# Kernel tuning notes

Measured on AMD Instinct MI355X. Metric: run time of the kernel, lower is better.

The kernel has to match this reference:

```python
import jax, jax.numpy as jnp
import numpy as np

H = 256          # LSTM hidden size
P = 1            # proj_size
L = 5            # num LSTM layers
T = 1000         # sequence length (forced by Linear(1000, 100))


def _uniform(key, shape, scale):
    return jax.random.uniform(key, shape, dtype=jnp.float32, minval=-scale, maxval=scale)


def setup_inputs() -> dict:
    key = jax.random.key(0)
    ks = jax.random.split(key, 16)
    B = 128
    s = 1.0 / np.sqrt(H)  # PyTorch LSTM init scale
    inp = {
        "x": jax.random.normal(ks[0], (B, T, 1), dtype=jnp.float32),
        # stacked LSTM params: layer input dim is 1 for all layers (input_size=1, proj_size=1)
        "Wih": _uniform(ks[1], (L, 4 * H, 1), s),
        "Whh": _uniform(ks[2], (L, 4 * H, P), s),
        "bih": _uniform(ks[3], (L, 4 * H), s),
        "bhh": _uniform(ks[4], (L, 4 * H), s),
        "Whr": _uniform(ks[5], (L, P, H), s),
        # MLP head
        "W1": _uniform(ks[6], (100, 1000), 1.0 / np.sqrt(1000)),
        "b1": _uniform(ks[7], (100,), 1.0 / np.sqrt(1000)),
        "W2": _uniform(ks[8], (100, 100), 0.1),
        "b2": _uniform(ks[9], (100,), 0.1),
        "W3": _uniform(ks[10], (100, 100), 0.1),
        "b3": _uniform(ks[11], (100,), 0.1),
        "W4": _uniform(ks[12], (1, 100), 0.1),
        "b4": _uniform(ks[13], (1,), 0.1),
    }
    return inp


def _lstm_layer(x_seq, Wih, Whh, bih, bhh, Whr):
    """One projected LSTM layer. x_seq: [B, T, in_dim] -> [B, T, P]."""
    B = x_seq.shape[0]
    # precompute input contribution for all timesteps: [B, T, 4H]
    gx = jnp.einsum('bti,gi->btg', x_seq, Wih) + bih + bhh
    gx = jnp.transpose(gx, (1, 0, 2))  # [T, B, 4H] for scan

    def step(carry, g_t):
        h, c = carry                      # h: [B, P], c: [B, H]
        gates = g_t + h @ Whh.T           # [B, 4H]
        i = jax.nn.sigmoid(gates[:, 0 * H:1 * H])
        f = jax.nn.sigmoid(gates[:, 1 * H:2 * H])
        g = jnp.tanh(gates[:, 2 * H:3 * H])
        o = jax.nn.sigmoid(gates[:, 3 * H:4 * H])
        c = f * c + i * g
        h = (o * jnp.tanh(c)) @ Whr.T     # projected hidden: [B, P]
        return (h, c), h

    h0 = jnp.zeros((B, P), x_seq.dtype)
    c0 = jnp.zeros((B, H), x_seq.dtype)
    _, hs = jax.lax.scan(step, (h0, c0), gx)  # hs: [T, B, P]
    return jnp.transpose(hs, (1, 0, 2))       # [B, T, P]


def reference(x, Wih, Whh, bih, bhh, Whr, W1, b1, W2, b2, W3, b3, W4, b4):
    out = x
    for l in range(L):  # fixed 5 stacked layers
        out = _lstm_layer(out, Wih[l], Whh[l], bih[l], bhh[l], Whr[l])
    out = out[:, :, 0]                      # squeeze -> [B, 1000]
    out = jax.nn.sigmoid(out @ W1.T + b1)   # linear1 + Sigmoid
    out = jax.nn.sigmoid(out @ W2.T + b2)   # linear2 + Sigmoid
    out = jax.nn.relu(out @ W3.T + b3)      # linear3 + ReLU
    out = out @ W4.T + b4                   # linear4 -> [B, 1]
    return out
```

## Files before the change

kernel.cpp:

```cpp
#include <hip/hip_runtime.h>


#define LAYERS 5
#define TT 1000
#define BATCH 128
#define CH 40
#define NCH (TT / CH)

#define LOG2E 1.4426950408889634f

__device__ __forceinline__ float fast_exp2(float x) {
#if __has_builtin(__builtin_amdgcn_exp2f)
  return __builtin_amdgcn_exp2f(x);
#else
  return __exp2f(x);
#endif
}
__device__ __forceinline__ float fast_rcp(float x) {
#if __has_builtin(__builtin_amdgcn_rcpf)
  return __builtin_amdgcn_rcpf(x);
#else
  return 1.0f / x;
#endif
}
__device__ __forceinline__ float fast_sigmoid(float z) {
  float e = fast_exp2(-LOG2E * z);
  return fast_rcp(1.0f + e);
}

template <int CTRL>
__device__ __forceinline__ float dpp_add(float v) {
  int moved = __builtin_amdgcn_update_dpp(0, __builtin_bit_cast(int, v),
                                          CTRL, 0xF, 0xF, false);
  return v + __builtin_bit_cast(float, moved);
}

__device__ __forceinline__ float wave_sum_uniform(float v) {
  v = dpp_add<0x128>(v);
  v = dpp_add<0x124>(v);
  v = dpp_add<0x122>(v);
  v = dpp_add<0x121>(v);
  v = dpp_add<0x142>(v);
  v = dpp_add<0x143>(v);
  return __builtin_bit_cast(float, __builtin_amdgcn_readlane(__builtin_bit_cast(int, v), 63));
}

__device__ __forceinline__ float lane_bcast(float v, int s) {
  return __builtin_bit_cast(float, __builtin_amdgcn_readlane(__builtin_bit_cast(int, v), s));
}

__global__ __launch_bounds__(64) void lstm_wave_kernel(
    const float* __restrict__ x,
    const float* __restrict__ Wih,
    const float* __restrict__ Whh,
    const float* __restrict__ bih,
    const float* __restrict__ bhh,
    const float* __restrict__ Whr,
    float* __restrict__ seq,
    int* __restrict__ flags)
{
  const int bid  = blockIdx.x;
  const int l    = bid >> 7;
  const int b    = bid & 127;
  const int lane = threadIdx.x;

  float wix[4][4], whx[4][4], gb[4][4], whr[4], cc[4];
  const int base = l * 1024;
#pragma unroll
  for (int g = 0; g < 4; ++g) {
    const float sc = (g == 2) ? (-2.0f * LOG2E) : (-LOG2E);
#pragma unroll
    for (int k = 0; k < 4; ++k) {
      int j = base + g * 256 + k * 64 + lane;
      wix[g][k] = Wih[j] * sc;
      whx[g][k] = Whh[j] * sc;
      gb[g][k]  = (bih[j] + bhh[j]) * sc;
    }
  }
#pragma unroll
  for (int k = 0; k < 4; ++k) {
    whr[k] = Whr[l * 256 + k * 64 + lane];
    cc[k] = 0.0f;
  }

  const float* in  = (l == 0) ? (x + b * TT) : (seq + ((l - 1) * BATCH + b) * TT);
  float*       out = seq + (l * BATCH + b) * TT;
  int*       my_flag = flags + l * BATCH + b;
  const int* in_flag = (l > 0) ? (flags + (l - 1) * BATCH + b) : (const int*)flags;

  float h = 0.0f;
  for (int c = 0; c < NCH; ++c) {
    if (l > 0) {
      while (__hip_atomic_load(in_flag, __ATOMIC_ACQUIRE,
                               __HIP_MEMORY_SCOPE_AGENT) <= c)
        __builtin_amdgcn_s_sleep(2);
    }
    float xv = 0.0f;
    if (lane < CH) {
      if (l == 0)
        xv = in[c * CH + lane];
      else
        xv = __hip_atomic_load(in + c * CH + lane, __ATOMIC_RELAXED,
                               __HIP_MEMORY_SCOPE_AGENT);
    }

    float outv = 0.0f;
#pragma unroll 2
    for (int s = 0; s < CH; ++s) {
      const float xs = lane_bcast(xv, s);

      float gx[4][4];
#pragma unroll
      for (int g = 0; g < 4; ++g)
#pragma unroll
        for (int k = 0; k < 4; ++k)
          gx[g][k] = fmaf(xs, wix[g][k], gb[g][k]);

      float E[4][4];
#pragma unroll
      for (int g = 0; g < 4; ++g)
#pragma unroll
        for (int k = 0; k < 4; ++k)
          E[g][k] = fast_exp2(fmaf(h, whx[g][k], gx[g][k]));

      float r0, r1, r2, r3;
      {
        float rr[4];
#pragma unroll
        for (int k = 0; k < 4; ++k) {
          float ig = fast_rcp(1.0f + E[0][k]);
          float fg = fast_rcp(1.0f + E[1][k]);
          float gg = fmaf(2.0f, fast_rcp(1.0f + E[2][k]), -1.0f);
          float og = fast_rcp(1.0f + E[3][k]);
          cc[k] = fmaf(fg, cc[k], ig * gg);
          float tE = fast_exp2(cc[k] * (-2.0f * LOG2E));
          float tc = fmaf(2.0f, fast_rcp(1.0f + tE), -1.0f);
          rr[k] = og * tc * whr[k];
        }
        r0 = rr[0]; r1 = rr[1]; r2 = rr[2]; r3 = rr[3];
      }
      float r = (r0 + r1) + (r2 + r3);

      h = wave_sum_uniform(r);
      if (lane == s) outv = h;
    }

    if (l < 4) {
      if (lane < CH)
        __hip_atomic_store(out + c * CH + lane, outv, __ATOMIC_RELAXED,
                           __HIP_MEMORY_SCOPE_AGENT);
      if (lane == 0)
        __hip_atomic_store(my_flag, c + 1, __ATOMIC_RELEASE,
                           __HIP_MEMORY_SCOPE_AGENT);
    } else {
      if (lane < CH) out[c * CH + lane] = outv;
    }
  }
}

__global__ __launch_bounds__(256) void mlp_head_kernel(
    const float* __restrict__ seq4,
    const float* __restrict__ W1, const float* __restrict__ b1,
    const float* __restrict__ W2, const float* __restrict__ b2,
    const float* __restrict__ W3, const float* __restrict__ b3,
    const float* __restrict__ W4, const float* __restrict__ b4,
    float* __restrict__ out)
{
  __shared__ float sx[TT];
  __shared__ float sh[100];
  __shared__ float sh2[100];
  __shared__ float part[100];
  __shared__ float red[4];

  const int b = blockIdx.x, tid = threadIdx.x;
  for (int i = tid; i < TT; i += 256) sx[i] = seq4[b * TT + i];
  __syncthreads();

  const int half = (tid >= 128) ? 1 : 0;
  const int oid  = half ? (tid - 128) : tid;
  float myacc = 0.0f;
  if (oid < 100) {
    const float* w  = W1 + oid * TT + half * 500;
    const float* xx = sx + half * 500;
    float a0 = 0.f, a1 = 0.f, a2 = 0.f, a3 = 0.f;
    for (int t0 = 0; t0 < 500; t0 += 4) {
      float4 v = *(const float4*)(w + t0);
      a0 = fmaf(v.x, xx[t0 + 0], a0);
      a1 = fmaf(v.y, xx[t0 + 1], a1);
      a2 = fmaf(v.z, xx[t0 + 2], a2);
      a3 = fmaf(v.w, xx[t0 + 3], a3);
    }
    myacc = (a0 + a1) + (a2 + a3);
    if (half) part[oid] = myacc;
  }
  __syncthreads();
  if (tid < 100) sh[tid] = fast_sigmoid(myacc + part[tid] + b1[tid]);
  __syncthreads();

  if (tid < 100) {
    float acc = b2[tid];
    const float* w = W2 + tid * 100;
    for (int k = 0; k < 100; ++k) acc += w[k] * sh[k];
    sh2[tid] = fast_sigmoid(acc);
  }
  __syncthreads();

  if (tid < 100) {
    float acc = b3[tid];
    const float* w = W3 + tid * 100;
    for (int k = 0; k < 100; ++k) acc += w[k] * sh2[k];
    sh[tid] = fmaxf(acc, 0.0f);
  }
  __syncthreads();

  float r = (tid < 100) ? sh[tid] * W4[tid] : 0.0f;
  {
    r = dpp_add<0x128>(r);
    r = dpp_add<0x124>(r);
    r = dpp_add<0x122>(r);
    r = dpp_add<0x121>(r);
    r = dpp_add<0x142>(r);
    r = dpp_add<0x143>(r);
    r = __builtin_bit_cast(float, __builtin_amdgcn_readlane(__builtin_bit_cast(int, r), 63));
  }
  if ((tid & 63) == 0) red[tid >> 6] = r;
  __syncthreads();
  if (tid == 0) out[b] = (red[0] + red[1]) + (red[2] + red[3]) + b4[0];
}

extern "C" void kernel_launch(void* const* d_in, const int* in_sizes, int n_in,
                              void* d_out, int out_size, void* d_ws, size_t ws_size,
                              hipStream_t stream) {
  const float* x   = (const float*)d_in[0];
  const float* Wih = (const float*)d_in[1];
  const float* Whh = (const float*)d_in[2];
  const float* bih = (const float*)d_in[3];
  const float* bhh = (const float*)d_in[4];
  const float* Whr = (const float*)d_in[5];
  const float* W1  = (const float*)d_in[6];
  const float* b1  = (const float*)d_in[7];
  const float* W2  = (const float*)d_in[8];
  const float* b2  = (const float*)d_in[9];
  const float* W3  = (const float*)d_in[10];
  const float* b3  = (const float*)d_in[11];
  const float* W4  = (const float*)d_in[12];
  const float* b4  = (const float*)d_in[13];

  float* seq   = (float*)d_ws;
  int*   flags = (int*)(seq + LAYERS * BATCH * TT);

  hipMemsetAsync(flags, 0, LAYERS * BATCH * sizeof(int), stream);
  lstm_wave_kernel<<<LAYERS * BATCH, 64, 0, stream>>>(x, Wih, Whh, bih, bhh, Whr,
                                                      seq, flags);
  mlp_head_kernel<<<BATCH, 256, 0, stream>>>(seq + 4 * BATCH * TT,
                                             W1, b1, W2, b2, W3, b3, W4, b4,
                                             (float*)d_out);
}
```

Before: 562.3 us.

## Spread each LSTM cell across four waves and fuse MLP head into layer-4 blocks

```diff
diff --git a/kernel.cpp b/kernel.cpp
--- a/kernel.cpp
+++ b/kernel.cpp
@@ -35,58 +35,70 @@
   return v + __builtin_bit_cast(float, moved);
 }
 
-__device__ __forceinline__ float wave_sum_uniform(float v) {
+__device__ __forceinline__ float wave_sum_hi(float v) {
   v = dpp_add<0x128>(v);
   v = dpp_add<0x124>(v);
   v = dpp_add<0x122>(v);
   v = dpp_add<0x121>(v);
   v = dpp_add<0x142>(v);
   v = dpp_add<0x143>(v);
-  return __builtin_bit_cast(float, __builtin_amdgcn_readlane(__builtin_bit_cast(int, v), 63));
+  return v;
 }
 
 __device__ __forceinline__ float lane_bcast(float v, int s) {
   return __builtin_bit_cast(float, __builtin_amdgcn_readlane(__builtin_bit_cast(int, v), s));
 }
 
-__global__ __launch_bounds__(64) void lstm_wave_kernel(
+__global__ __launch_bounds__(256) void lstm_fused_kernel(
     const float* __restrict__ x,
     const float* __restrict__ Wih,
     const float* __restrict__ Whh,
     const float* __restrict__ bih,
     const float* __restrict__ bhh,
     const float* __restrict__ Whr,
+    const float* __restrict__ W1, const float* __restrict__ b1,
+    const float* __restrict__ W2, const float* __restrict__ b2,
+    const float* __restrict__ W3, const float* __restrict__ b3,
+    const float* __restrict__ W4, const float* __restrict__ b4,
+    float* __restrict__ out,
     float* __restrict__ seq,
     int* __restrict__ flags)
 {
+  __shared__ __align__(16) float part[2][4];
+  __shared__ float sx[TT];
+  __shared__ float sh[100];
+  __shared__ float sh2[100];
+  __shared__ float partm[100];
+  __shared__ float red[4];
+
   const int bid  = blockIdx.x;
   const int l    = bid >> 7;
   const int b    = bid & 127;
-  const int lane = threadIdx.x;
-
-  float wix[4][4], whx[4][4], gb[4][4], whr[4], cc[4];
+  const int tid  = threadIdx.x;
+  const int wid  = tid >> 6;
+  const int lane = tid & 63;
+  const int e    = tid;
+
+  float wix[4], whx[4], gb[4];
   const int base = l * 1024;
 #pragma unroll
   for (int g = 0; g < 4; ++g) {
     const float sc = (g == 2) ? (-2.0f * LOG2E) : (-LOG2E);
-#pragma unroll
-    for (int k = 0; k < 4; ++k) {
-      int j = base + g * 256 + k * 64 + lane;
-      wix[g][k] = Wih[j] * sc;
-      whx[g][k] = Whh[j] * sc;
-      gb[g][k]  = (bih[j] + bhh[j]) * sc;
-    }
-  }
-#pragma unroll
-  for (int k = 0; k < 4; ++k) {
-    whr[k] = Whr[l * 256 + k * 64 + lane];
-    cc[k] = 0.0f;
-  }
-
-  const float* in  = (l == 0) ? (x + b * TT) : (seq + ((l - 1) * BATCH + b) * TT);
-  float*       out = seq + (l * BATCH + b) * TT;
+    int j = base + g * 256 + e;
+    wix[g] = Wih[j] * sc;
+    whx[g] = Whh[j] * sc;
+    gb[g]  = (bih[j] + bhh[j]) * sc;
+  }
+  const float whr = Whr[l * 256 + e];
+  float cc = 0.0f;
+
+  const float* in   = (l == 0) ? (x + b * TT) : (seq + ((l - 1) * BATCH + b) * TT);
+  float*       outp = seq + (l * BATCH + b) * TT;
   int*       my_flag = flags + l * BATCH + b;
   const int* in_flag = (l > 0) ? (flags + (l - 1) * BATCH + b) : (const int*)flags;
+
+  const float M4 = -4.0f * LOG2E;
+  const float P2 =  2.0f * LOG2E;
 
   float h = 0.0f;
   for (int c = 0; c < NCH; ++c) {
@@ -97,11 +109,9 @@
     }
     float xv = 0.0f;
     if (lane < CH) {
-      if (l == 0)
-        xv = in[c * CH + lane];
-      else
-        xv = __hip_atomic_load(in + c * CH + lane, __ATOMIC_RELAXED,
-                               __HIP_MEMORY_SCOPE_AGENT);
+      xv = (l == 0) ? in[c * CH + lane]
+                    : __hip_atomic_load(in + c * CH + lane, __ATOMIC_RELAXED,
+                                        __HIP_MEMORY_SCOPE_AGENT);
     }
 
     float outv = 0.0f;
@@ -109,71 +119,45 @@
     for (int s = 0; s < CH; ++s) {
       const float xs = lane_bcast(xv, s);
 
-      float gx[4][4];
-#pragma unroll
-      for (int g = 0; g < 4; ++g)
-#pragma unroll
-        for (int k = 0; k < 4; ++k)
-          gx[g][k] = fmaf(xs, wix[g][k], gb[g][k]);
-
-      float E[4][4];
-#pragma unroll
-      for (int g = 0; g < 4; ++g)
-#pragma unroll
-        for (int k = 0; k < 4; ++k)
-          E[g][k] = fast_exp2(fmaf(h, whx[g][k], gx[g][k]));
-
-      float r0, r1, r2, r3;
-      {
-        float rr[4];
-#pragma unroll
-        for (int k = 0; k < 4; ++k) {
-          float ig = fast_rcp(1.0f + E[0][k]);
-          float fg = fast_rcp(1.0f + E[1][k]);
-          float gg = fmaf(2.0f, fast_rcp(1.0f + E[2][k]), -1.0f);
-          float og = fast_rcp(1.0f + E[3][k]);
-          cc[k] = fmaf(fg, cc[k], ig * gg);
-          float tE = fast_exp2(cc[k] * (-2.0f * LOG2E));
-          float tc = fmaf(2.0f, fast_rcp(1.0f + tE), -1.0f);
-          rr[k] = og * tc * whr[k];
-        }
-        r0 = rr[0]; r1 = rr[1]; r2 = rr[2]; r3 = rr[3];
-      }
-      float r = (r0 + r1) + (r2 + r3);
-
-      h = wave_sum_uniform(r);
-      if (lane == s) outv = h;
-    }
-
-    if (l < 4) {
+      float p0 = fmaf(h, whx[0], fmaf(xs, wix[0], gb[0]));
+      float p1 = fmaf(h, whx[1], fmaf(xs, wix[1], gb[1]));
+      float p2 = fmaf(h, whx[2], fmaf(xs, wix[2], gb[2]));
+      float p3 = fmaf(h, whx[3], fmaf(xs, wix[3], gb[3]));
+      float E0 = fast_exp2(p0), E1 = fast_exp2(p1);
+      float E2 = fast_exp2(p2), E3 = fast_exp2(p3);
+      float R0 = fast_rcp(1.0f + E0);
+      float R1 = fast_rcp(1.0f + E1);
+      float R2 = fast_rcp(1.0f + E2);
+      float R3 = fast_rcp(1.0f + E3);
+      float gsc = fmaf(M4, R2, P2);
+      cc = fmaf(R1, cc, R0 * gsc);
+      float tR = fast_rcp(1.0f + fast_exp2(cc));
+      float ow = R3 * whr;
+      float r  = fmaf(ow + ow, tR, -ow);
+
+      float v = wave_sum_hi(r);
+      const int pr = s & 1;
+      if (lane == 63) part[pr][wid] = v;
+      __syncthreads();
+      const float4 pp = *(const float4*)part[pr];
+      h = (pp.x + pp.y) + (pp.z + pp.w);
+
+      if (wid == 0 && lane == s) outv = h;
+      if (l == 4 && tid == 0) sx[c * CH + s] = h;
+    }
+
+    if (l < 4 && wid == 0) {
       if (lane < CH)
-        __hip_atomic_store(out + c * CH + lane, outv, __ATOMIC_RELAXED,
+        __hip_atomic_store(outp + c * CH + lane, outv, __ATOMIC_RELAXED,
                            __HIP_MEMORY_SCOPE_AGENT);
       if (lane == 0)
         __hip_atomic_store(my_flag, c + 1, __ATOMIC_RELEASE,
                            __HIP_MEMORY_SCOPE_AGENT);
-    } else {
-      if (lane < CH) out[c * CH + lane] = outv;
-    }
-  }
-}
-
-__global__ __launch_bounds__(256) void mlp_head_kernel(
-    const float* __restrict__ seq4,
-    const float* __restrict__ W1, const float* __restrict__ b1,
-    const float* __restrict__ W2, const float* __restrict__ b2,
-    const float* __restrict__ W3, const float* __restrict__ b3,
-    const float* __restrict__ W4, const float* __restrict__ b4,
-    float* __restrict__ out)
-{
-  __shared__ float sx[TT];
-  __shared__ float sh[100];
-  __shared__ float sh2[100];
-  __shared__ float part[100];
-  __shared__ float red[4];
-
-  const int b = blockIdx.x, tid = threadIdx.x;
-  for (int i = tid; i < TT; i += 256) sx[i] = seq4[b * TT + i];
+    }
+  }
+
+  if (l != 4) return;
+
   __syncthreads();
 
   const int half = (tid >= 128) ? 1 : 0;
@@ -191,10 +175,10 @@
       a3 = fmaf(v.w, xx[t0 + 3], a3);
     }
     myacc = (a0 + a1) + (a2 + a3);
-    if (half) part[oid] = myacc;
-  }
-  __syncthreads();
-  if (tid < 100) sh[tid] = fast_sigmoid(myacc + part[tid] + b1[tid]);
+    if (half) partm[oid] = myacc;
+  }
+  __syncthreads();
+  if (tid < 100) sh[tid] = fast_sigmoid(myacc + partm[tid] + b1[tid]);
   __syncthreads();
 
   if (tid < 100) {
@@ -214,15 +198,13 @@
   __syncthreads();
 
   float r = (tid < 100) ? sh[tid] * W4[tid] : 0.0f;
-  {
-    r = dpp_add<0x128>(r);
-    r = dpp_add<0x124>(r);
-    r = dpp_add<0x122>(r);
-    r = dpp_add<0x121>(r);
-    r = dpp_add<0x142>(r);
-    r = dpp_add<0x143>(r);
-    r = __builtin_bit_cast(float, __builtin_amdgcn_readlane(__builtin_bit_cast(int, r), 63));
-  }
+  r = dpp_add<0x128>(r);
+  r = dpp_add<0x124>(r);
+  r = dpp_add<0x122>(r);
+  r = dpp_add<0x121>(r);
+  r = dpp_add<0x142>(r);
+  r = dpp_add<0x143>(r);
+  r = __builtin_bit_cast(float, __builtin_amdgcn_readlane(__builtin_bit_cast(int, r), 63));
   if ((tid & 63) == 0) red[tid >> 6] = r;
   __syncthreads();
   if (tid == 0) out[b] = (red[0] + red[1]) + (red[2] + red[3]) + b4[0];
@@ -250,9 +232,7 @@
   int*   flags = (int*)(seq + LAYERS * BATCH * TT);
 
   hipMemsetAsync(flags, 0, LAYERS * BATCH * sizeof(int), stream);
-  lstm_wave_kernel<<<LAYERS * BATCH, 64, 0, stream>>>(x, Wih, Whh, bih, bhh, Whr,
-                                                      seq, flags);
-  mlp_head_kernel<<<BATCH, 256, 0, stream>>>(seq + 4 * BATCH * TT,
-                                             W1, b1, W2, b2, W3, b3, W4, b4,
-                                             (float*)d_out);
-}
+  lstm_fused_kernel<<<LAYERS * BATCH, 256, 0, stream>>>(
+      x, Wih, Whh, bih, bhh, Whr, W1, b1, W2, b2, W3, b3, W4, b4,
+      (float*)d_out, seq, flags);
+}
```

Measured after the change: 843.6 us. 50.0% more time.

## Replace chunked flag handoff with per-timestep poisoned-value wavefront pipeline

Applied to the files above, without the earlier changes.

```diff
diff --git a/kernel.cpp b/kernel.cpp
--- a/kernel.cpp
+++ b/kernel.cpp
@@ -4,8 +4,7 @@
 #define LAYERS 5
 #define TT 1000
 #define BATCH 128
-#define CH 40
-#define NCH (TT / CH)
+#define POISON 0xFFFFFFFFu
 
 #define LOG2E 1.4426950408889634f
 
@@ -45,8 +44,8 @@
   return __builtin_bit_cast(float, __builtin_amdgcn_readlane(__builtin_bit_cast(int, v), 63));
 }
 
-__device__ __forceinline__ float lane_bcast(float v, int s) {
-  return __builtin_bit_cast(float, __builtin_amdgcn_readlane(__builtin_bit_cast(int, v), s));
+__device__ __forceinline__ unsigned int agent_load_u32(const unsigned int* p) {
+  return __hip_atomic_load(p, __ATOMIC_RELAXED, __HIP_MEMORY_SCOPE_AGENT);
 }
 
 __global__ __launch_bounds__(64) void lstm_wave_kernel(
@@ -56,8 +55,7 @@
     const float* __restrict__ bih,
     const float* __restrict__ bhh,
     const float* __restrict__ Whr,
-    float* __restrict__ seq,
-    int* __restrict__ flags)
+    float* __restrict__ seq)
 {
   const int bid  = blockIdx.x;
   const int l    = bid >> 7;
@@ -83,77 +81,61 @@
     cc[k] = 0.0f;
   }
 
-  const float* in  = (l == 0) ? (x + b * TT) : (seq + ((l - 1) * BATCH + b) * TT);
-  float*       out = seq + (l * BATCH + b) * TT;
-  int*       my_flag = flags + l * BATCH + b;
-  const int* in_flag = (l > 0) ? (flags + (l - 1) * BATCH + b) : (const int*)flags;
+  const unsigned int* in =
+      (const unsigned int*)((l == 0) ? (x + b * TT)
+                                     : (seq + ((l - 1) * BATCH + b) * TT));
+  float* outp = seq + (l * BATCH + b) * TT;
+
+  const float P2C = 2.0f * LOG2E;
+
+  unsigned int v0 = agent_load_u32(in);
+  while (v0 == POISON) v0 = agent_load_u32(in);
+  float xs = __builtin_bit_cast(float, v0);
+  unsigned int pf = agent_load_u32(in + 1);
 
   float h = 0.0f;
-  for (int c = 0; c < NCH; ++c) {
-    if (l > 0) {
-      while (__hip_atomic_load(in_flag, __ATOMIC_ACQUIRE,
-                               __HIP_MEMORY_SCOPE_AGENT) <= c)
-        __builtin_amdgcn_s_sleep(2);
-    }
-    float xv = 0.0f;
-    if (lane < CH) {
-      if (l == 0)
-        xv = in[c * CH + lane];
+#pragma unroll 2
+  for (int t = 0; t < TT; ++t) {
+    float E[4][4];
+#pragma unroll
+    for (int g = 0; g < 4; ++g)
+#pragma unroll
+      for (int k = 0; k < 4; ++k)
+        E[g][k] = fast_exp2(fmaf(h, whx[g][k], fmaf(xs, wix[g][k], gb[g][k])));
+
+    float rr[4];
+#pragma unroll
+    for (int k = 0; k < 4; ++k) {
+      float A0 = 1.0f + E[0][k];
+      float A1 = 1.0f + E[1][k];
+      float A2 = 1.0f + E[2][k];
+      float A3 = 1.0f + E[3][k];
+      float fg  = fast_rcp(A1);
+      float D02 = fast_rcp(A0 * A2);
+      float t2  = fmaf(P2C, E[2][k], -P2C);
+      cc[k] = fmaf(fg, cc[k], t2 * D02);
+      float Et  = fast_exp2(cc[k]);
+      float D3t = fast_rcp(A3 * (1.0f + Et));
+      rr[k] = fmaf(-Et, whr[k], whr[k]) * D3t;
+    }
+    float r = (rr[0] + rr[1]) + (rr[2] + rr[3]);
+
+    h = wave_sum_uniform(r);
+
+    if (lane == 0) {
+      if (l < 4)
+        __hip_atomic_store((unsigned int*)(outp + t),
+                           __builtin_bit_cast(unsigned int, h),
+                           __ATOMIC_RELAXED, __HIP_MEMORY_SCOPE_AGENT);
       else
-        xv = __hip_atomic_load(in + c * CH + lane, __ATOMIC_RELAXED,
-                               __HIP_MEMORY_SCOPE_AGENT);
-    }
-
-    float outv = 0.0f;
-#pragma unroll 2
-    for (int s = 0; s < CH; ++s) {
-      const float xs = lane_bcast(xv, s);
-
-      float gx[4][4];
-#pragma unroll
-      for (int g = 0; g < 4; ++g)
-#pragma unroll
-        for (int k = 0; k < 4; ++k)
-          gx[g][k] = fmaf(xs, wix[g][k], gb[g][k]);
-
-      float E[4][4];
-#pragma unroll
-      for (int g = 0; g < 4; ++g)
-#pragma unroll
-        for (int k = 0; k < 4; ++k)
-          E[g][k] = fast_exp2(fmaf(h, whx[g][k], gx[g][k]));
-
-      float r0, r1, r2, r3;
-      {
-        float rr[4];
-#pragma unroll
-        for (int k = 0; k < 4; ++k) {
-          float ig = fast_rcp(1.0f + E[0][k]);
-          float fg = fast_rcp(1.0f + E[1][k]);
-          float gg = fmaf(2.0f, fast_rcp(1.0f + E[2][k]), -1.0f);
-          float og = fast_rcp(1.0f + E[3][k]);
-          cc[k] = fmaf(fg, cc[k], ig * gg);
-          float tE = fast_exp2(cc[k] * (-2.0f * LOG2E));
-          float tc = fmaf(2.0f, fast_rcp(1.0f + tE), -1.0f);
-          rr[k] = og * tc * whr[k];
-        }
-        r0 = rr[0]; r1 = rr[1]; r2 = rr[2]; r3 = rr[3];
-      }
-      float r = (r0 + r1) + (r2 + r3);
-
-      h = wave_sum_uniform(r);
-      if (lane == s) outv = h;
-    }
-
-    if (l < 4) {
-      if (lane < CH)
-        __hip_atomic_store(out + c * CH + lane, outv, __ATOMIC_RELAXED,
-                           __HIP_MEMORY_SCOPE_AGENT);
-      if (lane == 0)
-        __hip_atomic_store(my_flag, c + 1, __ATOMIC_RELEASE,
-                           __HIP_MEMORY_SCOPE_AGENT);
-    } else {
-      if (lane < CH) out[c * CH + lane] = outv;
+        outp[t] = h;
+    }
+
+    if (t + 1 < TT) {
+      unsigned int v = pf;
+      while (v == POISON) v = agent_load_u32(in + t + 1);
+      xs = __builtin_bit_cast(float, v);
+      if (t + 2 < TT) pf = agent_load_u32(in + t + 2);
     }
   }
 }
@@ -214,15 +196,13 @@
   __syncthreads();
 
   float r = (tid < 100) ? sh[tid] * W4[tid] : 0.0f;
-  {
-    r = dpp_add<0x128>(r);
-    r = dpp_add<0x124>(r);
-    r = dpp_add<0x122>(r);
-    r = dpp_add<0x121>(r);
-    r = dpp_add<0x142>(r);
-    r = dpp_add<0x143>(r);
-    r = __builtin_bit_cast(float, __builtin_amdgcn_readlane(__builtin_bit_cast(int, r), 63));
-  }
+  r = dpp_add<0x128>(r);
+  r = dpp_add<0x124>(r);
+  r = dpp_add<0x122>(r);
+  r = dpp_add<0x121>(r);
+  r = dpp_add<0x142>(r);
+  r = dpp_add<0x143>(r);
+  r = __builtin_bit_cast(float, __builtin_amdgcn_readlane(__builtin_bit_cast(int, r), 63));
   if ((tid & 63) == 0) red[tid >> 6] = r;
   __syncthreads();
   if (tid == 0) out[b] = (red[0] + red[1]) + (red[2] + red[3]) + b4[0];
@@ -246,12 +226,11 @@
   const float* W4  = (const float*)d_in[12];
   const float* b4  = (const float*)d_in[13];
 
-  float* seq   = (float*)d_ws;
-  int*   flags = (int*)(seq + LAYERS * BATCH * TT);
-
-  hipMemsetAsync(flags, 0, LAYERS * BATCH * sizeof(int), stream);
-  lstm_wave_kernel<<<LAYERS * BATCH, 64, 0, stream>>>(x, Wih, Whh, bih, bhh, Whr,
-                                                      seq, flags);
+  float* seq = (float*)d_ws;
+
+  hipMemsetAsync(seq, 0xFF, (LAYERS - 1) * BATCH * TT * sizeof(float), stream);
+  lstm_wave_kernel<<<LAYERS * BATCH, 64, 0, stream>>>(x, Wih, Whh, bih, bhh,
+                                                      Whr, seq);
   mlp_head_kernel<<<BATCH, 256, 0, stream>>>(seq + 4 * BATCH * TT,
                                              W1, b1, W2, b2, W3, b3, W4, b4,
                                              (float*)d_out);
```

New measurement: 798.2 us. +41.9%, slower.
